# Kernel tuning notes

Measured on AMD Instinct MI355X. Metric: run time of the kernel, lower is better.

## Reference

```python
import jax, jax.numpy as jnp
import numpy as np

B, TIN, DIN = 128, 256, 64
H, TOUT, DOUT = 1024, 128, 128


def lstm_scan(x, Wi, Wh, b, h0, c0):
    """x: [B,T,D]. Returns (all hidden states [B,T,H], (h_T, c_T)).
    Gate order i, f, g, o (PyTorch convention)."""
    xg = jnp.einsum('btd,dg->btg', x, Wi) + b  # precompute input gates [B,T,4H]

    def step(carry, xg_t):
        h, c = carry
        g = xg_t + h @ Wh  # [B,4H]
        i, f, gg, o = jnp.split(g, 4, axis=-1)
        c = jax.nn.sigmoid(f) * c + jax.nn.sigmoid(i) * jnp.tanh(gg)
        h = jax.nn.sigmoid(o) * jnp.tanh(c)
        return (h, c), h

    (hT, cT), hs = jax.lax.scan(step, (h0, c0), jnp.swapaxes(xg, 0, 1))
    return jnp.swapaxes(hs, 0, 1), (hT, cT)


def setup_inputs() -> dict:
    key = jax.random.key(0)
    ks = jax.random.split(key, 7)
    s = lambda fan: 1.0 / np.sqrt(fan)
    return {
        'x': jax.random.normal(ks[0], (B, TIN, DIN), jnp.float32),
        'Wi1': jax.random.normal(ks[1], (DIN, 4 * H), jnp.float32) * s(H),
        'Wh1': jax.random.normal(ks[2], (H, 4 * H), jnp.float32) * s(H),
        'b1': jnp.zeros((4 * H,), jnp.float32),
        'Wi2': jax.random.normal(ks[3], (H, 4 * H), jnp.float32) * s(H),
        'Wh2': jax.random.normal(ks[4], (H, 4 * H), jnp.float32) * s(H),
        'b2': jnp.zeros((4 * H,), jnp.float32),
        'Wlin': jax.random.normal(ks[5], (H, DOUT), jnp.float32) * s(H),
        'blin': jnp.zeros((DOUT,), jnp.float32),
    }


def reference(x, Wi1, Wh1, b1, Wi2, Wh2, b2, Wlin, blin):
    h0 = jnp.zeros((x.shape[0], H), x.dtype)
    c0 = jnp.zeros((x.shape[0], H), x.dtype)
    # encoder: return_sequence=False, return_state=True
    hs1, (hT, cT) = lstm_scan(x, Wi1, Wh1, b1, h0, c0)
    t_last = hs1[:, -1, :]                      # [B,H]
    # time_repeat to decoder length
    z = jnp.broadcast_to(t_last[:, None, :], (x.shape[0], TOUT, H))
    # decoder initialized with encoder final state, returns full sequence
    hs2, _ = lstm_scan(z, Wi2, Wh2, b2, hT, cT)  # [B,TOUT,H]
    # linear head per timestep hidden -> output features
    return jnp.einsum('bth,hd->btd', hs2, Wlin) + blin
```

## Files before the change

### kernel.cpp

```cpp
#include <hip/hip_runtime.h>

#define NB   128
#define TIN  256
#define DIN  64
#define HD   1024
#define G4   4096
#define TOUTC 128
#define DOUTC 128

typedef _Float16 f16x8 __attribute__((ext_vector_type(8)));
typedef float    f32x4 __attribute__((ext_vector_type(4)));

#define FLAGS_OFF 0
#define HPP_OFF   65536
#define HS2_OFF   (HPP_OFF + 524288)
#define WLT_OFF   (HS2_OFF + 33554432)

__device__ __forceinline__ float sigm(float z) {
    return 1.0f / (1.0f + __expf(-z));
}
__device__ __forceinline__ float tanh_(float z) {
    float e = __expf(2.0f * z);
    return 1.0f - 2.0f / (e + 1.0f);
}

__device__ __forceinline__ void load_h8(const _Float16* p, f16x8 av[8]) {
    asm volatile(
        "global_load_dwordx4 %0, %8, off sc0 sc1\n\t"
        "global_load_dwordx4 %1, %8, off offset:64 sc0 sc1\n\t"
        "global_load_dwordx4 %2, %8, off offset:128 sc0 sc1\n\t"
        "global_load_dwordx4 %3, %8, off offset:192 sc0 sc1\n\t"
        "global_load_dwordx4 %4, %8, off offset:256 sc0 sc1\n\t"
        "global_load_dwordx4 %5, %8, off offset:320 sc0 sc1\n\t"
        "global_load_dwordx4 %6, %8, off offset:384 sc0 sc1\n\t"
        "global_load_dwordx4 %7, %8, off offset:448 sc0 sc1\n\t"
        "s_waitcnt vmcnt(0)"
        : "=&v"(av[0]), "=&v"(av[1]), "=&v"(av[2]), "=&v"(av[3]),
          "=&v"(av[4]), "=&v"(av[5]), "=&v"(av[6]), "=&v"(av[7])
        : "v"(p) : "memory");
}

__global__ void k_init(const float* __restrict__ Wlin, unsigned char* __restrict__ ws)
{
    int tid = blockIdx.x * blockDim.x + threadIdx.x;
    if (tid < 512) ((int*)(ws + FLAGS_OFF))[tid] = 0;
    _Float16* wlt = (_Float16*)(ws + WLT_OFF);
    for (int i = tid; i < DOUTC * HD; i += gridDim.x * blockDim.x) {
        int d = i >> 10, k = i & 1023;
        wlt[i] = (_Float16)Wlin[k * DOUTC + d];
    }
}

__global__ __launch_bounds__(512, 2)
void k_lstm(const float* __restrict__ x,   const float* __restrict__ Wi1,
            const float* __restrict__ Wh1, const float* __restrict__ b1,
            const float* __restrict__ Wi2, const float* __restrict__ Wh2,
            const float* __restrict__ b2,  unsigned char* __restrict__ ws)
{
    int* flagbase   = (int*)(ws + FLAGS_OFF);
    _Float16* hpp   = (_Float16*)(ws + HPP_OFF);
    _Float16* hs2   = (_Float16*)(ws + HS2_OFF);

    const int tid  = threadIdx.x;
    const int lane = tid & 63;
    const int w    = tid >> 6;
    const int t    = w & 1;
    const int ks   = w >> 1;
    const int gid  = blockIdx.x;
    const int g    = gid & 7;
    const int p    = gid >> 3;
    const int u0   = p * 32 + t * 16;
    const int l15  = lane & 15;
    const int lhi  = lane >> 4;
    const int grow = g * 16 + l15;
    const int kq   = ks << 8;

    __shared__ float parts[2][3][2][4][16][17];
    __shared__ float xg2s[2][4][16][17];
    __shared__ int   token_s;

    if (tid == 0) token_s = 0;
    __syncthreads();
    volatile int* tokp = &token_s;

    f16x8 wB[8][4];
    f16x8 wX[2][4];
    float bias4[4];
    f32x4 cst = {0.f, 0.f, 0.f, 0.f};

    {
        const float* W = Wh1;
        #pragma unroll
        for (int kk = 0; kk < 8; ++kk)
        #pragma unroll
        for (int ct = 0; ct < 4; ++ct) {
            const int col = ct * HD + u0 + l15;
            const int kb  = kq + kk * 32 + lhi * 8;
            f16x8 v;
            #pragma unroll
            for (int e = 0; e < 8; ++e) v[e] = (_Float16)W[(kb + e) * G4 + col];
            wB[kk][ct] = v;
        }
    }
    if (ks == 1) {
        #pragma unroll
        for (int kk = 0; kk < 2; ++kk)
        #pragma unroll
        for (int ct = 0; ct < 4; ++ct) {
            const int col = ct * HD + u0 + l15;
            const int kb  = kk * 32 + lhi * 8;
            f16x8 v;
            #pragma unroll
            for (int e = 0; e < 8; ++e) v[e] = (_Float16)Wi1[(kb + e) * G4 + col];
            wX[kk][ct] = v;
        }
    }
    if (ks == 0) {
        #pragma unroll
        for (int ct = 0; ct < 4; ++ct) bias4[ct] = b1[ct * HD + u0 + l15];
    }

    const int* pollbase = flagbase + g * 64 + lane;
    int* myslot         = flagbase + g * 64 + (p >> 3) * 16 + (p & 7) * 2 + t;

    int  tok  = 0;
    bool dead = false;

    auto WAIT = [&](int target) {
        if (w == 0) {
            if (!dead && tok < target) {
                long it = 0;
                for (;;) {
                    int v;
                    asm volatile("global_load_dword %0, %1, off sc0 sc1\n\ts_waitcnt vmcnt(0)"
                                 : "=v"(v) : "v"(pollbase) : "memory");
                    if (__all(v >= target)) break;
                    __builtin_amdgcn_s_sleep(1);
                    if (++it > (1L << 21)) { dead = true; break; }
                }
            }
            if (tok < target) { tok = target; if (lane == 0) *tokp = target; }
        } else {
            if (!dead) {
                long it = 0;
                while (*tokp < target) {
                    __builtin_amdgcn_s_sleep(1);
                    if (++it > (1L << 24)) { dead = true; break; }
                }
            }
        }
    };

    #pragma unroll 1
    for (int s = 0; s < 384; ++s) {
        if (s == 256) {
            WAIT(256);
            f32x4 acc[4];
            #pragma unroll
            for (int ct = 0; ct < 4; ++ct) acc[ct] = {0.f,0.f,0.f,0.f};
            const _Float16* hprev = hpp + 1 * NB * HD;
            f16x8 av[8];
            load_h8(hprev + grow * HD + kq + lhi * 8, av);
            #pragma unroll
            for (int kk = 0; kk < 8; ++kk) {
                const int kb = kq + kk * 32 + lhi * 8;
                #pragma unroll
                for (int ct = 0; ct < 4; ++ct) {
                    const int col = ct * HD + u0 + l15;
                    f16x8 bb;
                    #pragma unroll
                    for (int e = 0; e < 8; ++e) bb[e] = (_Float16)Wi2[(kb + e) * G4 + col];
                    acc[ct] = __builtin_amdgcn_mfma_f32_16x16x32_f16(av[kk], bb, acc[ct], 0, 0, 0);
                }
            }
            if (ks > 0) {
                #pragma unroll
                for (int ct = 0; ct < 4; ++ct)
                #pragma unroll
                for (int i = 0; i < 4; ++i)
                    parts[0][ks - 1][t][ct][l15][lhi * 4 + i] = acc[ct][i];
            }
            __syncthreads();
            if (ks == 0) {
                #pragma unroll
                for (int ct = 0; ct < 4; ++ct) {
                    #pragma unroll
                    for (int j = 0; j < 3; ++j)
                    #pragma unroll
                    for (int i = 0; i < 4; ++i)
                        acc[ct][i] += parts[0][j][t][ct][l15][lhi * 4 + i];
                    const float bv = b2[ct * HD + u0 + l15];
                    #pragma unroll
                    for (int i = 0; i < 4; ++i)
                        xg2s[t][ct][l15][lhi * 4 + i] = acc[ct][i] + bv;
                }
            }
            __syncthreads();
            {
                const float* W = Wh2;
                #pragma unroll
                for (int kk = 0; kk < 8; ++kk)
                #pragma unroll
                for (int ct = 0; ct < 4; ++ct) {
                    const int col = ct * HD + u0 + l15;
                    const int kb  = kq + kk * 32 + lhi * 8;
                    f16x8 v;
                    #pragma unroll
                    for (int e = 0; e < 8; ++e) v[e] = (_Float16)W[(kb + e) * G4 + col];
                    wB[kk][ct] = v;
                }
            }
        }

        const int  par = s & 1;
        const bool l2  = (s >= 256);

        if (s > 0) WAIT(s);

        f32x4 acc[4];
        if (ks == 0) {
            if (!l2) {
                #pragma unroll
                for (int ct = 0; ct < 4; ++ct)
                    acc[ct] = {bias4[ct], bias4[ct], bias4[ct], bias4[ct]};
            } else {
                #pragma unroll
                for (int ct = 0; ct < 4; ++ct)
                #pragma unroll
                for (int i = 0; i < 4; ++i)
                    acc[ct][i] = xg2s[t][ct][l15][lhi * 4 + i];
            }
        } else {
            #pragma unroll
            for (int ct = 0; ct < 4; ++ct) acc[ct] = {0.f,0.f,0.f,0.f};
        }

        if (s > 0) {
            const _Float16* hprev = hpp + ((s + 1) & 1) * NB * HD;
            f16x8 av[8];
            load_h8(hprev + grow * HD + kq + lhi * 8, av);
            #pragma unroll
            for (int kk = 0; kk < 8; ++kk) {
                #pragma unroll
                for (int ct = 0; ct < 4; ++ct)
                    acc[ct] = __builtin_amdgcn_mfma_f32_16x16x32_f16(av[kk], wB[kk][ct], acc[ct], 0, 0, 0);
            }
        }
        if (!l2 && ks == 1) {
            const float* xp = x + (grow * TIN + s) * DIN;
            #pragma unroll
            for (int kk = 0; kk < 2; ++kk) {
                const int kb = kk * 32 + lhi * 8;
                f32x4 x0 = *(const f32x4*)(xp + kb);
                f32x4 x1 = *(const f32x4*)(xp + kb + 4);
                f16x8 a;
                #pragma unroll
                for (int e = 0; e < 4; ++e) { a[e] = (_Float16)x0[e]; a[e + 4] = (_Float16)x1[e]; }
                #pragma unroll
                for (int ct = 0; ct < 4; ++ct)
                    acc[ct] = __builtin_amdgcn_mfma_f32_16x16x32_f16(a, wX[kk][ct], acc[ct], 0, 0, 0);
            }
        }

        if (ks > 0) {
            #pragma unroll
            for (int ct = 0; ct < 4; ++ct)
            #pragma unroll
            for (int i = 0; i < 4; ++i)
                parts[par][ks - 1][t][ct][l15][lhi * 4 + i] = acc[ct][i];
        }
        __syncthreads();

        if (ks == 0) {
            #pragma unroll
            for (int ct = 0; ct < 4; ++ct)
            #pragma unroll
            for (int j = 0; j < 3; ++j)
            #pragma unroll
            for (int i = 0; i < 4; ++i)
                acc[ct][i] += parts[par][j][t][ct][l15][lhi * 4 + i];

            _Float16* hout = hpp + par * NB * HD;
            unsigned  hb[4];
            _Float16  hfs[4];
            #pragma unroll
            for (int i = 0; i < 4; ++i) {
                const float ig = sigm(acc[0][i]);
                const float fg = sigm(acc[1][i]);
                const float gg = tanh_(acc[2][i]);
                const float og = sigm(acc[3][i]);
                const float cn = fg * cst[i] + ig * gg;
                cst[i] = cn;
                const float hn = og * tanh_(cn);
                const _Float16 hf = (_Float16)hn;
                hfs[i] = hf;
                hb[i] = (unsigned)__builtin_bit_cast(unsigned short, hf);
            }
            _Float16* p01 = hout + (g * 16 + lhi * 4) * HD + u0 + l15;
            _Float16* p23 = p01 + 2 * HD;
            asm volatile(
                "global_store_short %0, %2, off sc0 sc1\n\t"
                "global_store_short %0, %3, off offset:2048 sc0 sc1\n\t"
                "global_store_short %1, %4, off sc0 sc1\n\t"
                "global_store_short %1, %5, off offset:2048 sc0 sc1\n\t"
                "s_waitcnt vmcnt(0)"
                :: "v"(p01), "v"(p23), "v"(hb[0]), "v"(hb[1]), "v"(hb[2]), "v"(hb[3])
                : "memory");
            if (lane == 0) {
                const int val = s + 1;
                asm volatile("global_store_dword %0, %1, off sc0 sc1"
                             :: "v"(myslot), "v"(val) : "memory");
            }
            if (l2) {
                #pragma unroll
                for (int i = 0; i < 4; ++i) {
                    const int row = g * 16 + lhi * 4 + i;
                    hs2[((s - 256) * NB + row) * HD + u0 + l15] = hfs[i];
                }
            }
        }
    }
}

__global__ __launch_bounds__(512, 2)
void k_out(const unsigned char* __restrict__ ws, const float* __restrict__ blin,
           float* __restrict__ out)
{
    const _Float16* hs2 = (const _Float16*)(ws + HS2_OFF);
    const _Float16* wlt = (const _Float16*)(ws + WLT_OFF);
    const int tid  = threadIdx.x;
    const int lane = tid & 63;
    const int l15  = lane & 15, lhi = lane >> 4;
    const int w    = tid >> 6;
    const int wb   = w & 3, wd = w >> 2;
    const int t    = blockIdx.x >> 1;
    const int dh   = blockIdx.x & 1;
    const int b0   = wb * 32;
    const int d0   = dh * 64 + wd * 32;

    f32x4 acc[2][2];
    #pragma unroll
    for (int a_ = 0; a_ < 2; ++a_)
    #pragma unroll
    for (int b_ = 0; b_ < 2; ++b_) acc[a_][b_] = {0.f,0.f,0.f,0.f};

    #pragma unroll 4
    for (int kk = 0; kk < 32; ++kk) {
        const int kb = kk * 32 + lhi * 8;
        f16x8 a0 = *(const f16x8*)(hs2 + (t * NB + b0 + l15) * HD + kb);
        f16x8 a1 = *(const f16x8*)(hs2 + (t * NB + b0 + 16 + l15) * HD + kb);
        f16x8 q0 = *(const f16x8*)(wlt + (d0 + l15) * HD + kb);
        f16x8 q1 = *(const f16x8*)(wlt + (d0 + 16 + l15) * HD + kb);
        acc[0][0] = __builtin_amdgcn_mfma_f32_16x16x32_f16(a0, q0, acc[0][0], 0, 0, 0);
        acc[0][1] = __builtin_amdgcn_mfma_f32_16x16x32_f16(a0, q1, acc[0][1], 0, 0, 0);
        acc[1][0] = __builtin_amdgcn_mfma_f32_16x16x32_f16(a1, q0, acc[1][0], 0, 0, 0);
        acc[1][1] = __builtin_amdgcn_mfma_f32_16x16x32_f16(a1, q1, acc[1][1], 0, 0, 0);
    }
    #pragma unroll
    for (int bi = 0; bi < 2; ++bi)
    #pragma unroll
    for (int dj = 0; dj < 2; ++dj) {
        const int dcol = d0 + dj * 16 + l15;
        const float bv = blin[dcol];
        #pragma unroll
        for (int i = 0; i < 4; ++i) {
            const int row = b0 + bi * 16 + lhi * 4 + i;
            out[(row * TOUTC + t) * DOUTC + dcol] = acc[bi][dj][i] + bv;
        }
    }
}

extern "C" void kernel_launch(void* const* d_in, const int* in_sizes, int n_in,
                              void* d_out, int out_size, void* d_ws, size_t ws_size,
                              hipStream_t stream)
{
    const float* x    = (const float*)d_in[0];
    const float* Wi1  = (const float*)d_in[1];
    const float* Wh1  = (const float*)d_in[2];
    const float* b1   = (const float*)d_in[3];
    const float* Wi2  = (const float*)d_in[4];
    const float* Wh2  = (const float*)d_in[5];
    const float* b2   = (const float*)d_in[6];
    const float* Wlin = (const float*)d_in[7];
    const float* blin = (const float*)d_in[8];
    unsigned char* ws = (unsigned char*)d_ws;
    float* out = (float*)d_out;

    k_init<<<256, 256, 0, stream>>>(Wlin, ws);
    k_lstm<<<256, 512, 0, stream>>>(x, Wi1, Wh1, b1, Wi2, Wh2, b2, ws);
    k_out <<<256, 512, 0, stream>>>(ws, blin, out);
}
```

Measured before the change: 3.367 ms.

## Use per-timestep hidden-state ring buffer with cached loads when workspace allows

Replaces the double-buffered hidden-state exchange with a ring buffer holding one slot per timestep. Each slot is written only once, so readers can use ordinary cached loads instead of the sc0 sc1 system-coherent loads. The decoder ring slots also serve directly as the input to the output projection, which removes the separate hs2 store. This needs a much larger workspace; if that is not available, the kernel falls back to the old path.

```diff
diff --git a/kernel.cpp b/kernel.cpp
--- a/kernel.cpp
+++ b/kernel.cpp
@@ -15,6 +15,9 @@
 #define HPP_OFF   65536
 #define HS2_OFF   (HPP_OFF + 524288)
 #define WLT_OFF   (HS2_OFF + 33554432)
+#define RING_OFF  34603008ULL
+#define SLOT_ELT  (NB * HD)
+#define RING_NEED (RING_OFF + 384ULL * (SLOT_ELT * 2))
 
 __device__ __forceinline__ float sigm(float z) {
     return 1.0f / (1.0f + __expf(-z));
@@ -24,7 +27,7 @@
     return 1.0f - 2.0f / (e + 1.0f);
 }
 
-__device__ __forceinline__ void load_h8(const _Float16* p, f16x8 av[8]) {
+__device__ __forceinline__ void load_h8_llc(const _Float16* p, f16x8 av[8]) {
     asm volatile(
         "global_load_dwordx4 %0, %8, off sc0 sc1\n\t"
         "global_load_dwordx4 %1, %8, off offset:64 sc0 sc1\n\t"
@@ -40,6 +43,12 @@
         : "v"(p) : "memory");
 }
 
+__device__ __forceinline__ void load_h8_cached(const _Float16* p, f16x8 av[8]) {
+    #pragma unroll
+    for (int kk = 0; kk < 8; ++kk)
+        av[kk] = *(const f16x8*)(p + kk * 32);
+}
+
 __global__ void k_init(const float* __restrict__ Wlin, unsigned char* __restrict__ ws)
 {
     int tid = blockIdx.x * blockDim.x + threadIdx.x;
@@ -51,6 +60,7 @@
     }
 }
 
+template<bool RING>
 __global__ __launch_bounds__(512, 2)
 void k_lstm(const float* __restrict__ x,   const float* __restrict__ Wi1,
             const float* __restrict__ Wh1, const float* __restrict__ b1,
@@ -60,6 +70,7 @@
     int* flagbase   = (int*)(ws + FLAGS_OFF);
     _Float16* hpp   = (_Float16*)(ws + HPP_OFF);
     _Float16* hs2   = (_Float16*)(ws + HS2_OFF);
+    _Float16* ring  = (_Float16*)(ws + RING_OFF);
 
     const int tid  = threadIdx.x;
     const int lane = tid & 63;
@@ -149,6 +160,7 @@
                 }
             }
         }
+        asm volatile("" ::: "memory");
     };
 
     #pragma unroll 1
@@ -158,9 +170,11 @@
             f32x4 acc[4];
             #pragma unroll
             for (int ct = 0; ct < 4; ++ct) acc[ct] = {0.f,0.f,0.f,0.f};
-            const _Float16* hprev = hpp + 1 * NB * HD;
+            const _Float16* hprev = RING ? (ring + 255 * SLOT_ELT)
+                                         : (hpp + 1 * NB * HD);
             f16x8 av[8];
-            load_h8(hprev + grow * HD + kq + lhi * 8, av);
+            if (RING) load_h8_cached(hprev + grow * HD + kq + lhi * 8, av);
+            else      load_h8_llc   (hprev + grow * HD + kq + lhi * 8, av);
             #pragma unroll
             for (int kk = 0; kk < 8; ++kk) {
                 const int kb = kq + kk * 32 + lhi * 8;
@@ -236,9 +250,11 @@
         }
 
         if (s > 0) {
-            const _Float16* hprev = hpp + ((s + 1) & 1) * NB * HD;
+            const _Float16* hprev = RING ? (ring + (s - 1) * SLOT_ELT)
+                                         : (hpp + ((s + 1) & 1) * NB * HD);
             f16x8 av[8];
-            load_h8(hprev + grow * HD + kq + lhi * 8, av);
+            if (RING) load_h8_cached(hprev + grow * HD + kq + lhi * 8, av);
+            else      load_h8_llc   (hprev + grow * HD + kq + lhi * 8, av);
             #pragma unroll
             for (int kk = 0; kk < 8; ++kk) {
                 #pragma unroll
@@ -280,7 +296,6 @@
             for (int i = 0; i < 4; ++i)
                 acc[ct][i] += parts[par][j][t][ct][l15][lhi * 4 + i];
 
-            _Float16* hout = hpp + par * NB * HD;
             unsigned  hb[4];
             _Float16  hfs[4];
             #pragma unroll
@@ -296,6 +311,8 @@
                 hfs[i] = hf;
                 hb[i] = (unsigned)__builtin_bit_cast(unsigned short, hf);
             }
+            _Float16* hout = RING ? (ring + s * SLOT_ELT)
+                                  : (hpp + par * NB * HD);
             _Float16* p01 = hout + (g * 16 + lhi * 4) * HD + u0 + l15;
             _Float16* p23 = p01 + 2 * HD;
             asm volatile(
@@ -311,7 +328,7 @@
                 asm volatile("global_store_dword %0, %1, off sc0 sc1"
                              :: "v"(myslot), "v"(val) : "memory");
             }
-            if (l2) {
+            if (!RING && l2) {
                 #pragma unroll
                 for (int i = 0; i < 4; ++i) {
                     const int row = g * 16 + lhi * 4 + i;
@@ -323,11 +340,9 @@
 }
 
 __global__ __launch_bounds__(512, 2)
-void k_out(const unsigned char* __restrict__ ws, const float* __restrict__ blin,
-           float* __restrict__ out)
+void k_out(const _Float16* __restrict__ hsb, const _Float16* __restrict__ wlt,
+           const float* __restrict__ blin, float* __restrict__ out)
 {
-    const _Float16* hs2 = (const _Float16*)(ws + HS2_OFF);
-    const _Float16* wlt = (const _Float16*)(ws + WLT_OFF);
     const int tid  = threadIdx.x;
     const int lane = tid & 63;
     const int l15  = lane & 15, lhi = lane >> 4;
@@ -347,8 +362,8 @@
     #pragma unroll 4
     for (int kk = 0; kk < 32; ++kk) {
         const int kb = kk * 32 + lhi * 8;
-        f16x8 a0 = *(const f16x8*)(hs2 + (t * NB + b0 + l15) * HD + kb);
-        f16x8 a1 = *(const f16x8*)(hs2 + (t * NB + b0 + 16 + l15) * HD + kb);
+        f16x8 a0 = *(const f16x8*)(hsb + (t * NB + b0 + l15) * HD + kb);
+        f16x8 a1 = *(const f16x8*)(hsb + (t * NB + b0 + 16 + l15) * HD + kb);
         f16x8 q0 = *(const f16x8*)(wlt + (d0 + l15) * HD + kb);
         f16x8 q1 = *(const f16x8*)(wlt + (d0 + 16 + l15) * HD + kb);
         acc[0][0] = __builtin_amdgcn_mfma_f32_16x16x32_f16(a0, q0, acc[0][0], 0, 0, 0);
@@ -386,7 +401,17 @@
     unsigned char* ws = (unsigned char*)d_ws;
     float* out = (float*)d_out;
 
+    const bool ring = (ws_size >= RING_NEED);
+
     k_init<<<256, 256, 0, stream>>>(Wlin, ws);
-    k_lstm<<<256, 512, 0, stream>>>(x, Wi1, Wh1, b1, Wi2, Wh2, b2, ws);
-    k_out <<<256, 512, 0, stream>>>(ws, blin, out);
-}
+    if (ring)
+        k_lstm<true ><<<256, 512, 0, stream>>>(x, Wi1, Wh1, b1, Wi2, Wh2, b2, ws);
+    else
+        k_lstm<false><<<256, 512, 0, stream>>>(x, Wi1, Wh1, b1, Wi2, Wh2, b2, ws);
+
+    const _Float16* hsb = ring
+        ? (const _Float16*)(ws + RING_OFF) + 256ULL * SLOT_ELT
+        : (const _Float16*)(ws + HS2_OFF);
+    const _Float16* wlt = (const _Float16*)(ws + WLT_OFF);
+    k_out<<<256, 512, 0, stream>>>(hsb, wlt, blin, out);
+}
```

Result: slower. 3.986 ms (+18.4%).
